# Optimization experiments

Hardware: AMD Instinct MI355X
Metric: run time of the kernel (lower is better)

## Reference

```python
import jax, jax.numpy as jnp
import numpy as np

COST_CLASS = 1.0
COST_BBOX = 1.0
COST_GIOU = 1.0


def box_cxcywh_to_xyxy(b):
    cx, cy, w, h = jnp.split(b, 4, axis=-1)
    return jnp.concatenate([cx - 0.5 * w, cy - 0.5 * h, cx + 0.5 * w, cy + 0.5 * h], axis=-1)


def generalized_box_iou(b1, b2):
    # b1: [N,4] xyxy, b2: [M,4] xyxy -> [N,M]
    a1 = (b1[:, 2] - b1[:, 0]) * (b1[:, 3] - b1[:, 1])  # [N]
    a2 = (b2[:, 2] - b2[:, 0]) * (b2[:, 3] - b2[:, 1])  # [M]
    lt = jnp.maximum(b1[:, None, :2], b2[None, :, :2])  # [N,M,2]
    rb = jnp.minimum(b1[:, None, 2:], b2[None, :, 2:])
    wh = jnp.clip(rb - lt, 0.0)
    inter = wh[..., 0] * wh[..., 1]
    union = a1[:, None] + a2[None, :] - inter
    iou = inter / union
    lt_e = jnp.minimum(b1[:, None, :2], b2[None, :, :2])
    rb_e = jnp.maximum(b1[:, None, 2:], b2[None, :, 2:])
    wh_e = jnp.clip(rb_e - lt_e, 0.0)
    area = wh_e[..., 0] * wh_e[..., 1]
    return iou - (area - union) / area


def setup_inputs() -> dict:
    key = jax.random.key(0)
    k1, k2, k3, k4, k5 = jax.random.split(key, 5)
    bs, nq, d, total_tgt = 16, 900, 256, 1600
    return {
        "pred_logits": jax.random.normal(k1, (bs, nq, d), dtype=jnp.float32),
        "pred_boxes": jax.random.uniform(k2, (bs, nq, 4), dtype=jnp.float32),
        "tgt_embs": jax.random.normal(k3, (total_tgt, d), dtype=jnp.float32),
        "tgt_bbox": jax.random.uniform(k4, (total_tgt, 4), dtype=jnp.float32),
        "tgt_sizes": jax.random.randint(k5, (bs,), 0, 100, dtype=jnp.int32),  # only used by host-side LSA
    }


def reference(pred_logits, pred_boxes, tgt_embs, tgt_bbox, tgt_sizes):
    # Returns the sigmoid-squashed cost volume C [bs, num_queries, total_tgt];
    # scipy linear_sum_assignment over tgt_sizes splits is a host-side step.
    bs, nq = pred_logits.shape[:2]
    out_prob = pred_logits.reshape(bs * nq, -1)
    out_bbox = pred_boxes.reshape(bs * nq, 4)
    out_prob = out_prob / jnp.linalg.norm(out_prob, axis=-1, keepdims=True)
    cost_class = jax.nn.relu(out_prob @ tgt_embs.T)                    # [N,M]
    cost_bbox = jnp.sum(jnp.abs(out_bbox[:, None, :] - tgt_bbox[None, :, :]), axis=-1)  # L1 cdist
    cost_giou = -generalized_box_iou(box_cxcywh_to_xyxy(out_bbox), box_cxcywh_to_xyxy(tgt_bbox))
    C = COST_BBOX * cost_bbox + COST_CLASS * cost_class + COST_GIOU * cost_giou
    return jax.nn.sigmoid(C.reshape(bs, nq, -1))
```

## Files before the change

kernel.cpp:

```cpp
#include <hip/hip_runtime.h>

#define N_ROWS 14400
#define M_COLS 1600
#define KDIM   256
#define GRID_X 25
#define GRID_Y 113
#define NWG    (GRID_X * GRID_Y)

typedef __attribute__((ext_vector_type(8))) short bf16x8;
typedef __attribute__((ext_vector_type(4))) float f32x4;

__device__ __forceinline__ short f2bf(float x) {
  union { float f; unsigned u; } v; v.f = x;
  unsigned r = v.u + 0x7FFFu + ((v.u >> 16) & 1u);
  return (short)(r >> 16);
}

__device__ __forceinline__ void gload_lds16(const void* g, void* l) {
  __builtin_amdgcn_global_load_lds(
      (const __attribute__((address_space(1))) void*)g,
      (__attribute__((address_space(3))) void*)l, 16, 0, 0);
}

__global__ __launch_bounds__(256) void prep_kernel(
    const float* __restrict__ logits, const float* __restrict__ embs,
    short* __restrict__ probB, short* __restrict__ embB) {
  const int row = blockIdx.x * 4 + (threadIdx.x >> 6);
  const int lane = threadIdx.x & 63;
  if (row < N_ROWS) {
    const float4 x = ((const float4*)(logits + (size_t)row * KDIM))[lane];
    float s = x.x * x.x + x.y * x.y + x.z * x.z + x.w * x.w;
#pragma unroll
    for (int o = 32; o > 0; o >>= 1) s += __shfl_xor(s, o, 64);
    const float scale = __builtin_amdgcn_rsqf(s);
    short4 o4;
    o4.x = f2bf(x.x * scale); o4.y = f2bf(x.y * scale);
    o4.z = f2bf(x.z * scale); o4.w = f2bf(x.w * scale);
    ((short4*)(probB + (size_t)row * KDIM))[lane] = o4;
  } else {
    const int r = row - N_ROWS;
    const float4 x = ((const float4*)(embs + (size_t)r * KDIM))[lane];
    short4 o4;
    o4.x = f2bf(x.x); o4.y = f2bf(x.y); o4.z = f2bf(x.z); o4.w = f2bf(x.w);
    ((short4*)(embB + (size_t)r * KDIM))[lane] = o4;
  }
}

__global__ __launch_bounds__(256) void cost_kernel(
    const short* __restrict__ probB, const short* __restrict__ embB,
    const float* __restrict__ pbox, const float* __restrict__ tbox,
    float* __restrict__ out) {
  __shared__ short As[128 * 64];
  __shared__ short Bs[64 * 64];
  __shared__ f32x4 rowcc[128], rowxy[128];
  __shared__ f32x4 colcc[64],  colxy[64];
  float* const tbuf = (float*)As;

  const int t = threadIdx.x;
  const int lane = t & 63;
  const int wid = t >> 6;
  const int wr = wid >> 1;
  const int wc = wid & 1;

  const int orig = blockIdx.x;
  const int xcd = orig & 7;
  const int rem = orig >> 3;
  const int q = NWG >> 3, r = NWG & 7;
  const int wgid = (xcd < r ? xcd * (q + 1) : r * (q + 1) + (xcd - r) * q) + rem;
  const int bx = wgid % GRID_X;
  const int by = wgid / GRID_X;
  const int rowBase = by * 128;
  const int colBase = bx * 64;

  if (t < 128) {
    const int idx = rowBase + t;
    const int ci = idx < N_ROWS ? idx : N_ROWS - 1;
    const float4 bb = ((const float4*)pbox)[ci];
    rowcc[t] = (f32x4){bb.x, bb.y, bb.z, bb.w};
    rowxy[t] = (f32x4){fmaf(-0.5f, bb.z, bb.x), fmaf(-0.5f, bb.w, bb.y),
                       fmaf(0.5f, bb.z, bb.x), fmaf(0.5f, bb.w, bb.y)};
  } else if (t < 192) {
    const int c = t - 128;
    const float4 bb = ((const float4*)tbox)[colBase + c];
    colcc[c] = (f32x4){bb.x, bb.y, bb.z, bb.w};
    colxy[c] = (f32x4){fmaf(-0.5f, bb.z, bb.x), fmaf(-0.5f, bb.w, bb.y),
                       fmaf(0.5f, bb.z, bb.x), fmaf(0.5f, bb.w, bb.y)};
  }

  f32x4 acc[4][2];
#pragma unroll
  for (int i = 0; i < 4; ++i)
#pragma unroll
    for (int j = 0; j < 2; ++j) acc[i][j] = (f32x4){0.f, 0.f, 0.f, 0.f};

  const int swz = (lane & 7) ^ (lane >> 3);
  const int rbase = wid * 8 + (lane >> 3);

  for (int kt = 0; kt < 4; ++kt) {
    const int k0 = kt * 64 + swz * 8;
#pragma unroll
    for (int i = 0; i < 4; ++i) {
      int gr = rowBase + i * 32 + rbase;
      if (gr > N_ROWS - 1) gr = N_ROWS - 1;
      gload_lds16(probB + (size_t)gr * KDIM + k0, As + (i * 32 + wid * 8) * 64);
    }
#pragma unroll
    for (int i = 0; i < 2; ++i) {
      const int gc = colBase + i * 32 + rbase;
      gload_lds16(embB + (size_t)gc * KDIM + k0, Bs + (i * 32 + wid * 8) * 64);
    }
    __syncthreads();
#pragma unroll
    for (int kk = 0; kk < 2; ++kk) {
      bf16x8 af[4], bfr[2];
      const int g = kk * 4 + (lane >> 4);
#pragma unroll
      for (int mi = 0; mi < 4; ++mi) {
        const int row = wr * 64 + mi * 16 + (lane & 15);
        af[mi] = *(const bf16x8*)(As + row * 64 + ((g ^ (row & 7)) * 8));
      }
#pragma unroll
      for (int ni = 0; ni < 2; ++ni) {
        const int row = wc * 32 + ni * 16 + (lane & 15);
        bfr[ni] = *(const bf16x8*)(Bs + row * 64 + ((g ^ (row & 7)) * 8));
      }
#pragma unroll
      for (int mi = 0; mi < 4; ++mi)
#pragma unroll
        for (int ni = 0; ni < 2; ++ni)
          acc[mi][ni] = __builtin_amdgcn_mfma_f32_16x16x32_bf16(
              af[mi], bfr[ni], acc[mi][ni], 0, 0, 0);
    }
    __syncthreads();
  }

  const float LOG2E = 1.44269504f;
  const int jr = (lane >> 4) * 4;
  const int lc = lane & 15;
  f32x4 c0v[2], c1v[2];
  float cav[2];
#pragma unroll
  for (int ni = 0; ni < 2; ++ni) {
    const int cloc = wc * 32 + ni * 16 + lc;
    c0v[ni] = colcc[cloc];
    c1v[ni] = colxy[cloc];
    cav[ni] = c0v[ni][2] * c0v[ni][3];
  }

#pragma unroll
  for (int mi = 0; mi < 4; ++mi) {
    float* const tb = tbuf + (mi & 1) * 2176;
#pragma unroll
    for (int j = 0; j < 4; ++j) {
      const int rloc = wr * 64 + mi * 16 + jr + j;
      const f32x4 r0 = rowcc[rloc];
      const f32x4 r1 = rowxy[rloc];
      const float ra = r0[2] * r0[3];
#pragma unroll
      for (int ni = 0; ni < 2; ++ni) {
        const f32x4 c0 = c0v[ni], c1 = c1v[ni];
        const float cc = fmaxf(acc[mi][ni][j], 0.0f);
        const float l1 = fabsf(r0[0] - c0[0]) + fabsf(r0[1] - c0[1]) +
                         fabsf(r0[2] - c0[2]) + fabsf(r0[3] - c0[3]);
        const float iwx = fminf(r1[2], c1[2]) - fmaxf(r1[0], c1[0]);
        const float iwy = fminf(r1[3], c1[3]) - fmaxf(r1[1], c1[1]);
        const float iw = fmaxf(iwx, 0.f);
        const float ih = fmaxf(iwy, 0.f);
        const float inter = iw * ih;
        const float uni = ra + cav[ni] - inter;
        const float ex = (r0[2] + c0[2]) - iwx;
        const float ey = (r0[3] + c0[3]) - iwy;
        const float earea = ex * ey;
        const float num = fmaf(uni, uni, inter * earea);
        const float Cv = fmaf(-num, __builtin_amdgcn_rcpf(uni * earea),
                              l1 + cc + 1.0f);
        const float sg = __builtin_amdgcn_rcpf(
            1.0f + __builtin_amdgcn_exp2f(-LOG2E * Cv));
        tb[(wr * 16 + jr + j) * 68 + wc * 32 + ni * 16 + lc] = sg;
      }
    }
    asm volatile("s_waitcnt lgkmcnt(0)" ::: "memory");
    __builtin_amdgcn_s_barrier();
#pragma unroll
    for (int rr = 0; rr < 2; ++rr) {
      const int rch = rr * 16 + (t >> 4);
      const int c4 = (t & 15) * 4;
      const f32x4 v = *(const f32x4*)(tb + rch * 68 + c4);
      const int grow = rowBase + ((rch < 16) ? (mi * 16 + rch)
                                             : (64 + mi * 16 + (rch - 16)));
      if (grow < N_ROWS)
        __builtin_nontemporal_store(
            v, (f32x4*)(out + (size_t)grow * M_COLS + colBase + c4));
    }
  }
}

extern "C" void kernel_launch(void* const* d_in, const int* in_sizes, int n_in,
                              void* d_out, int out_size, void* d_ws, size_t ws_size,
                              hipStream_t stream) {
  const float* logits = (const float*)d_in[0];
  const float* pbox   = (const float*)d_in[1];
  const float* embs   = (const float*)d_in[2];
  const float* tbox   = (const float*)d_in[3];
  float* out = (float*)d_out;

  short* probB = (short*)d_ws;
  short* embB  = probB + (size_t)N_ROWS * KDIM;

  prep_kernel<<<(N_ROWS + M_COLS) / 4, 256, 0, stream>>>(logits, embs, probB, embB);

  cost_kernel<<<NWG, 256, 0, stream>>>(probB, embB, pbox, tbox, out);
}
```

Before: 48.11 us.

## Split fused cost kernel into GEMM writing fp16 scores and separate epilogue

The fused GEMM+epilogue kernel is split into a GEMM kernel that stores fp16 class scores in a fragment-native layout to workspace, and a separate elementwise epilogue kernel that computes the box costs, GIoU and sigmoid with fully coalesced 8-wide loads and stores. Column box terms are precomputed once by an extra prep block in a structure-of-arrays layout. The aim is to take the epilogue's LDS staging and barriers out of the GEMM and let both stages run at full occupancy. In exchange it adds an extra ~46MB round trip of fp16 scores through memory plus an extra launch, and rounds the class cost to fp16. The old fused path remains as a fallback when the workspace is too small.

```diff
diff --git a/kernel.cpp b/kernel.cpp
--- a/kernel.cpp
+++ b/kernel.cpp
@@ -7,8 +7,13 @@
 #define GRID_Y 113
 #define NWG    (GRID_X * GRID_Y)
 
+#define COLD_OFF   8192000ull
+#define SC_OFF     8249600ull
+#define WS_NEED    54534400ull
+
 typedef __attribute__((ext_vector_type(8))) short bf16x8;
 typedef __attribute__((ext_vector_type(4))) float f32x4;
+typedef __attribute__((ext_vector_type(8))) unsigned short u16x8;
 
 __device__ __forceinline__ short f2bf(float x) {
   union { float f; unsigned u; } v; v.f = x;
@@ -24,7 +29,24 @@
 
 __global__ __launch_bounds__(256) void prep_kernel(
     const float* __restrict__ logits, const float* __restrict__ embs,
-    short* __restrict__ probB, short* __restrict__ embB) {
+    const float* __restrict__ tbox,
+    short* __restrict__ probB, short* __restrict__ embB,
+    float* __restrict__ colD) {
+  if (blockIdx.x >= (N_ROWS + M_COLS) / 4) {
+    for (int c = threadIdx.x; c < M_COLS; c += 256) {
+      const float4 bb = ((const float4*)tbox)[c];
+      colD[0 * M_COLS + c] = fmaf(-0.5f, bb.z, bb.x);
+      colD[1 * M_COLS + c] = fmaf(-0.5f, bb.w, bb.y);
+      colD[2 * M_COLS + c] = fmaf(0.5f, bb.z, bb.x);
+      colD[3 * M_COLS + c] = fmaf(0.5f, bb.w, bb.y);
+      colD[4 * M_COLS + c] = bb.x;
+      colD[5 * M_COLS + c] = bb.y;
+      colD[6 * M_COLS + c] = bb.z;
+      colD[7 * M_COLS + c] = bb.w;
+      colD[8 * M_COLS + c] = bb.z * bb.w;
+    }
+    return;
+  }
   const int row = blockIdx.x * 4 + (threadIdx.x >> 6);
   const int lane = threadIdx.x & 63;
   if (row < N_ROWS) {
@@ -43,6 +65,151 @@
     short4 o4;
     o4.x = f2bf(x.x); o4.y = f2bf(x.y); o4.z = f2bf(x.z); o4.w = f2bf(x.w);
     ((short4*)(embB + (size_t)r * KDIM))[lane] = o4;
+  }
+}
+
+__global__ __launch_bounds__(256) void gemm_kernel(
+    const short* __restrict__ probB, const short* __restrict__ embB,
+    unsigned short* __restrict__ sc) {
+  __shared__ short As[128 * 64];
+  __shared__ short Bs[64 * 64];
+
+  const int t = threadIdx.x;
+  const int lane = t & 63;
+  const int wid = t >> 6;
+  const int wr = wid >> 1;
+  const int wc = wid & 1;
+
+  const int orig = blockIdx.x;
+  const int xcd = orig & 7;
+  const int rem = orig >> 3;
+  const int q = NWG >> 3, r = NWG & 7;
+  const int wgid = (xcd < r ? xcd * (q + 1) : r * (q + 1) + (xcd - r) * q) + rem;
+  const int bx = wgid % GRID_X;
+  const int by = wgid / GRID_X;
+  const int rowBase = by * 128;
+  const int colBase = bx * 64;
+
+  f32x4 acc[4][2];
+#pragma unroll
+  for (int i = 0; i < 4; ++i)
+#pragma unroll
+    for (int j = 0; j < 2; ++j) acc[i][j] = (f32x4){0.f, 0.f, 0.f, 0.f};
+
+  const int swz = (lane & 7) ^ (lane >> 3);
+  const int rbase = wid * 8 + (lane >> 3);
+
+  for (int kt = 0; kt < 4; ++kt) {
+    const int k0 = kt * 64 + swz * 8;
+#pragma unroll
+    for (int i = 0; i < 4; ++i) {
+      int gr = rowBase + i * 32 + rbase;
+      if (gr > N_ROWS - 1) gr = N_ROWS - 1;
+      gload_lds16(probB + (size_t)gr * KDIM + k0, As + (i * 32 + wid * 8) * 64);
+    }
+#pragma unroll
+    for (int i = 0; i < 2; ++i) {
+      const int gc = colBase + i * 32 + rbase;
+      gload_lds16(embB + (size_t)gc * KDIM + k0, Bs + (i * 32 + wid * 8) * 64);
+    }
+    __syncthreads();
+#pragma unroll
+    for (int kk = 0; kk < 2; ++kk) {
+      bf16x8 af[4], bfr[2];
+      const int g = kk * 4 + (lane >> 4);
+#pragma unroll
+      for (int mi = 0; mi < 4; ++mi) {
+        const int row = wr * 64 + mi * 16 + (lane & 15);
+        af[mi] = *(const bf16x8*)(As + row * 64 + ((g ^ (row & 7)) * 8));
+      }
+#pragma unroll
+      for (int ni = 0; ni < 2; ++ni) {
+        const int row = wc * 32 + ni * 16 + (lane & 15);
+        bfr[ni] = *(const bf16x8*)(Bs + row * 64 + ((g ^ (row & 7)) * 8));
+      }
+#pragma unroll
+      for (int mi = 0; mi < 4; ++mi)
+#pragma unroll
+        for (int ni = 0; ni < 2; ++ni)
+          acc[mi][ni] = __builtin_amdgcn_mfma_f32_16x16x32_bf16(
+              af[mi], bfr[ni], acc[mi][ni], 0, 0, 0);
+    }
+    __syncthreads();
+  }
+
+  const size_t sbase = ((size_t)wgid * 4 + wid) * 2048;
+#pragma unroll
+  for (int mi = 0; mi < 4; ++mi)
+#pragma unroll
+    for (int ni = 0; ni < 2; ++ni)
+#pragma unroll
+      for (int j = 0; j < 4; ++j) {
+        union { _Float16 h; unsigned short u; } cv;
+        cv.h = (_Float16)acc[mi][ni][j];
+        sc[sbase + mi * 512 + ni * 256 + j * 64 + lane] = cv.u;
+      }
+}
+
+__global__ __launch_bounds__(256) void epi_kernel(
+    const unsigned short* __restrict__ sc, const float* __restrict__ pbox,
+    const float* __restrict__ colD, float* __restrict__ out) {
+  const int tid = blockIdx.x * 256 + threadIdx.x;
+  const int row = tid / 200;
+  const int c0 = (tid - row * 200) * 8;
+
+  const int by = row >> 7, ry = row & 127;
+  const int wr = ry >> 6, mi = (ry >> 4) & 3, qq = (ry >> 2) & 3, j = ry & 3;
+  const int bx = c0 >> 6, wc = (c0 >> 5) & 1, ni = (c0 >> 4) & 1, l0 = c0 & 15;
+  const int lane = qq * 16 + l0;
+  const int wid = wr * 2 + wc;
+  const size_t sidx = ((size_t)(by * GRID_X + bx) * 4 + wid) * 2048 +
+                      mi * 512 + ni * 256 + j * 64 + lane;
+  const u16x8 sv = *(const u16x8*)(sc + sidx);
+
+  const float4 rb = ((const float4*)pbox)[row];
+  const float rx1 = fmaf(-0.5f, rb.z, rb.x);
+  const float ry1 = fmaf(-0.5f, rb.w, rb.y);
+  const float rx2 = fmaf(0.5f, rb.z, rb.x);
+  const float ry2 = fmaf(0.5f, rb.w, rb.y);
+  const float ra = rb.z * rb.w;
+  const float LOG2E = 1.44269504f;
+
+#pragma unroll
+  for (int h = 0; h < 2; ++h) {
+    const int ch = c0 + h * 4;
+    const f32x4 X1 = *(const f32x4*)(colD + 0 * M_COLS + ch);
+    const f32x4 Y1 = *(const f32x4*)(colD + 1 * M_COLS + ch);
+    const f32x4 X2 = *(const f32x4*)(colD + 2 * M_COLS + ch);
+    const f32x4 Y2 = *(const f32x4*)(colD + 3 * M_COLS + ch);
+    const f32x4 CX = *(const f32x4*)(colD + 4 * M_COLS + ch);
+    const f32x4 CY = *(const f32x4*)(colD + 5 * M_COLS + ch);
+    const f32x4 CW = *(const f32x4*)(colD + 6 * M_COLS + ch);
+    const f32x4 CH = *(const f32x4*)(colD + 7 * M_COLS + ch);
+    const f32x4 CA = *(const f32x4*)(colD + 8 * M_COLS + ch);
+    f32x4 res;
+#pragma unroll
+    for (int k = 0; k < 4; ++k) {
+      union { unsigned short u; _Float16 hh; } cv;
+      cv.u = sv[h * 4 + k];
+      const float cc = fmaxf((float)cv.hh, 0.0f);
+      const float l1 = fabsf(rb.x - CX[k]) + fabsf(rb.y - CY[k]) +
+                       fabsf(rb.z - CW[k]) + fabsf(rb.w - CH[k]);
+      const float iwx = fminf(rx2, X2[k]) - fmaxf(rx1, X1[k]);
+      const float iwy = fminf(ry2, Y2[k]) - fmaxf(ry1, Y1[k]);
+      const float iw = fmaxf(iwx, 0.f);
+      const float ih = fmaxf(iwy, 0.f);
+      const float inter = iw * ih;
+      const float uni = ra + CA[k] - inter;
+      const float ex = (rb.z + CW[k]) - iwx;
+      const float ey = (rb.w + CH[k]) - iwy;
+      const float earea = ex * ey;
+      const float num = fmaf(uni, uni, inter * earea);
+      const float Cv = fmaf(-num, __builtin_amdgcn_rcpf(uni * earea),
+                            l1 + cc + 1.0f);
+      res[k] = __builtin_amdgcn_rcpf(
+          1.0f + __builtin_amdgcn_exp2f(-LOG2E * Cv));
+    }
+    __builtin_nontemporal_store(res, (f32x4*)(out + (size_t)row * M_COLS + ch));
   }
 }
 
@@ -206,8 +373,18 @@
 
   short* probB = (short*)d_ws;
   short* embB  = probB + (size_t)N_ROWS * KDIM;
-
-  prep_kernel<<<(N_ROWS + M_COLS) / 4, 256, 0, stream>>>(logits, embs, probB, embB);
-
-  cost_kernel<<<NWG, 256, 0, stream>>>(probB, embB, pbox, tbox, out);
-}
+  float* colD  = (float*)((char*)d_ws + COLD_OFF);
+  unsigned short* sc = (unsigned short*)((char*)d_ws + SC_OFF);
+
+  if (ws_size >= WS_NEED) {
+    prep_kernel<<<(N_ROWS + M_COLS) / 4 + 1, 256, 0, stream>>>(
+        logits, embs, tbox, probB, embB, colD);
+    gemm_kernel<<<NWG, 256, 0, stream>>>(probB, embB, sc);
+    epi_kernel<<<(N_ROWS * M_COLS) / (8 * 256), 256, 0, stream>>>(
+        sc, pbox, colD, out);
+  } else {
+    prep_kernel<<<(N_ROWS + M_COLS) / 4, 256, 0, stream>>>(
+        logits, embs, tbox, probB, embB, colD);
+    cost_kernel<<<NWG, 256, 0, stream>>>(probB, embB, pbox, tbox, out);
+  }
+}
```

Result: slower. 85.15 us (+77.0%).
